# Kernel tuning notes

Hardware: AMD Instinct MI355X
Metric: run time of the kernel (lower is better)

The kernel has to match this reference:

```python
import jax, jax.numpy as jnp
import numpy as np

B, S, F, O = 128, 8, 32, 16  # batch, board_size, in_features, out_features
D = 2 * S - 1                # diff_size = 15 relative offsets per axis


def setup_inputs() -> dict:
    key = jax.random.key(0)
    k1, k2, k3 = jax.random.split(key, 3)
    inp = jax.random.normal(k1, (B, S, S, F), dtype=jnp.float32)
    # torch.nn.Bilinear init: U(-1/sqrt(in1_features), 1/sqrt(in1_features))
    bound = 1.0 / np.sqrt(F)
    W = jax.random.uniform(k2, (D, D, O, F, F), jnp.float32, -bound, bound)
    b = jax.random.uniform(k3, (D, D, O), jnp.float32, -bound, bound)
    return {"inp": inp, "W": W, "b": b}


def reference(inp, W, b):
    # inp: (B, S, S, F); W: (D, D, O, F, F); b: (D, D, O)
    s = inp.shape[1]
    idx = jnp.arange(s)
    # offset index: off[a, bb] = bb - a + (s - 1), in [0, 2s-2]
    off = idx[None, :] - idx[:, None] + (s - 1)  # (S, S)
    # gather per-pair bilinear weights: Wg[ax, bx, ay, by] = W[bx-ax+7, by-ay+7]
    Wg = W[off[:, :, None, None], off[None, None, :, :]]  # (S,S,S,S,O,F,F)
    bg = b[off[:, :, None, None], off[None, None, :, :]]  # (S,S,S,S,O) [ax,bx,ay,by]
    # out[b, ax, ay, bx, by, o] = a_i W_oij b_j + bias_o
    out = jnp.einsum('bxyi,xXyYoij,bXYj->bxyXYo', inp, Wg, inp)
    out = out + bg.transpose(0, 2, 1, 3, 4)[None]  # bias to [ax,ay,bx,by,o]
    return out
```

## Files before the change

### kernel.cpp

```cpp
#include <hip/hip_runtime.h>

typedef _Float16 f16;
typedef _Float16 f16x8 __attribute__((ext_vector_type(8)));
typedef float f32x4 __attribute__((ext_vector_type(4)));
typedef unsigned int u32;
typedef const __attribute__((address_space(1))) u32* gas1_t;
typedef __attribute__((address_space(3))) u32* las3_t;

#define WGRAN 460800
#define IGRAN 32768

__global__ __launch_bounds__(256) void convert_kernel(
    const float* __restrict__ W, const float* __restrict__ inp,
    f16* __restrict__ W_h, f16* __restrict__ inp_h)
{
    const int g = blockIdx.x * 256 + threadIdx.x;
    if (g < WGRAN) {
        const int dxdy = g >> 11;
        const int r = g & 2047;
        const int i = r >> 6, o = (r >> 2) & 15, quad = r & 3;
        const float* src = W + (size_t)dxdy * 16384 + o * 1024 + i * 32 + quad * 8;
        const float4 v0 = *(const float4*)src;
        const float4 v1 = *(const float4*)(src + 4);
        f16x8 h = { (f16)v0.x, (f16)v0.y, (f16)v0.z, (f16)v0.w,
                    (f16)v1.x, (f16)v1.y, (f16)v1.z, (f16)v1.w };
        *(f16x8*)(W_h + (size_t)g * 8) = h;
    } else {
        const int k = g - WGRAN;
        const float* src = inp + (size_t)k * 8;
        const float4 v0 = *(const float4*)src;
        const float4 v1 = *(const float4*)(src + 4);
        f16x8 h = { (f16)v0.x, (f16)v0.y, (f16)v0.z, (f16)v0.w,
                    (f16)v1.x, (f16)v1.y, (f16)v1.z, (f16)v1.w };
        *(f16x8*)(inp_h + (size_t)k * 8) = h;
    }
}

__global__ __launch_bounds__(256, 2) void rel_mfma7(
    const f16* __restrict__ W_h,
    const f16* __restrict__ inp_h,
    const float* __restrict__ bias,
    float* __restrict__ out)
{
    extern __shared__ __align__(16) f16 Wl[];

    const int hw = blockIdx.x;
    const int X = hw & 7, y = (hw >> 3) & 7, x = (hw >> 6) & 7;
    const int dx = X - x + 7;

    const int t = threadIdx.x;
    const int lane = t & 63;
    const int wave = t >> 6;
    const int quad = lane >> 4;
    const int m = lane & 15;

    const f16* wbase = W_h + (size_t)(dx * 15 + 7 - y) * 16384;

    #pragma unroll
    for (int it = 0; it < 8; ++it) {
        const int idx = (it * 256 + t) * 8;
        __builtin_amdgcn_global_load_lds((gas1_t)(wbase + idx),
                                         (las3_t)&Wl[idx], 16, 0, 0);
    }

    f16x8 a0[4], a1[4], c0[8], c1[8];
    const int b0 = wave * 32 + m;
    const int b1 = b0 + 16;
    {
        const f16* ar0 = inp_h + ((b0 * 8 + x) * 8 + y) * 32;
        const f16* ar1 = inp_h + ((b1 * 8 + x) * 8 + y) * 32;
        #pragma unroll
        for (int g = 0; g < 4; ++g) {
            a0[g] = *(const f16x8*)(ar0 + g * 8);
            a1[g] = *(const f16x8*)(ar1 + g * 8);
        }
        const f16* cr0 = inp_h + (b0 * 8 + X) * 256 + quad * 8;
        const f16* cr1 = inp_h + (b1 * 8 + X) * 256 + quad * 8;
        #pragma unroll
        for (int Yi = 0; Yi < 8; ++Yi) {
            c0[Yi] = *(const f16x8*)(cr0 + Yi * 32);
            c1[Yi] = *(const f16x8*)(cr1 + Yi * 32);
        }
    }

    __syncthreads();

    const int bid_base = ((x * 8 + y) * 8 + X) * 8;

    #pragma unroll
    for (int Y = 0; Y < 8; ++Y) {
        const int cur = Y & 1;

        if (Y < 7) {
            const f16* nbase = wbase + (size_t)(Y + 1) * 16384;
            f16* ldst = Wl + (cur ^ 1) * 16384;
            #pragma unroll
            for (int it = 0; it < 8; ++it) {
                const int idx = (it * 256 + t) * 8;
                __builtin_amdgcn_global_load_lds((gas1_t)(nbase + idx),
                                                 (las3_t)&ldst[idx], 16, 0, 0);
            }
        }
        __builtin_amdgcn_sched_barrier(0);

        f32x4 acc0 = {0.f, 0.f, 0.f, 0.f};
        f32x4 acc1 = {0.f, 0.f, 0.f, 0.f};
        const f16* wl = Wl + cur * 16384 + m * 32 + quad * 8;
        f16x8 bfrag = *(const f16x8*)(wl);
        #pragma unroll
        for (int kb = 0; kb < 32; ++kb) {
            const f16x8 bcur = bfrag;
            if (kb < 31)
                bfrag = *(const f16x8*)(wl + (kb + 1) * 512);
            const f16 av0 = a0[kb >> 3][kb & 7];
            const f16 av1 = a1[kb >> 3][kb & 7];
            const f16x8 af0 = c0[Y] * av0;
            const f16x8 af1 = c1[Y] * av1;
            acc0 = __builtin_amdgcn_mfma_f32_16x16x32_f16(af0, bcur, acc0, 0, 0, 0);
            acc1 = __builtin_amdgcn_mfma_f32_16x16x32_f16(af1, bcur, acc1, 0, 0, 0);
        }

        const int dxdy = dx * 15 + (Y - y + 7);
        const int bid = bid_base + Y;
        const float bv = bias[dxdy * 16 + m];
        #pragma unroll
        for (int r = 0; r < 4; ++r) {
            const int bb = wave * 32 + quad * 4 + r;
            out[((size_t)bb * 4096 + bid) * 16 + m]        = acc0[r] + bv;
            out[((size_t)(bb + 16) * 4096 + bid) * 16 + m] = acc1[r] + bv;
        }

        if (Y < 7) {
            __builtin_amdgcn_sched_barrier(0);
            asm volatile("s_waitcnt vmcnt(8)" ::: "memory");
            __builtin_amdgcn_s_barrier();
            __builtin_amdgcn_sched_barrier(0);
        }
    }
}

extern "C" void kernel_launch(void* const* d_in, const int* in_sizes, int n_in,
                              void* d_out, int out_size, void* d_ws, size_t ws_size,
                              hipStream_t stream)
{
    const float* inp  = (const float*)d_in[0];
    const float* W    = (const float*)d_in[1];
    const float* bias = (const float*)d_in[2];
    float* out = (float*)d_out;

    f16* W_h   = (f16*)d_ws;
    f16* inp_h = (f16*)d_ws + (size_t)WGRAN * 8;

    hipLaunchKernelGGL(convert_kernel, dim3((WGRAN + IGRAN) / 256), dim3(256), 0,
                       stream, W, inp, W_h, inp_h);
    hipLaunchKernelGGL(rel_mfma7, dim3(512), dim3(256), 65536, stream,
                       W_h, inp_h, bias, out);
}
```

Measured before the change: 105.0 us.

## Batch LDS weight reads into phases with barriers and MFMA priority boost

Restructures the inner K loop into four phases. Each phase first loads eight B-fragments from LDS, then issues the MFMAs between workgroup barriers under raised wave priority (s_setprio), which gives the waves a ping-pong style schedule. The next weight tile's global-to-LDS prefetch is now issued after the first phase's LDS reads instead of before the compute. Bias values are preloaded into registers up front. Extra barriers per phase add sync cost and more live registers, which risks occupancy at the 2-blocks launch bound.

```diff
diff --git a/kernel.cpp b/kernel.cpp
--- a/kernel.cpp
+++ b/kernel.cpp
@@ -36,7 +36,7 @@
     }
 }
 
-__global__ __launch_bounds__(256, 2) void rel_mfma7(
+__global__ __launch_bounds__(256, 2) void rel_mfma8(
     const f16* __restrict__ W_h,
     const f16* __restrict__ inp_h,
     const float* __restrict__ bias,
@@ -64,6 +64,7 @@
     }
 
     f16x8 a0[4], a1[4], c0[8], c1[8];
+    float bv[8];
     const int b0 = wave * 32 + m;
     const int b1 = b0 + 16;
     {
@@ -80,6 +81,7 @@
         for (int Yi = 0; Yi < 8; ++Yi) {
             c0[Yi] = *(const f16x8*)(cr0 + Yi * 32);
             c1[Yi] = *(const f16x8*)(cr1 + Yi * 32);
+            bv[Yi] = bias[(dx * 15 + (Yi - y + 7)) * 16 + m];
         }
     }
 
@@ -90,44 +92,51 @@
     #pragma unroll
     for (int Y = 0; Y < 8; ++Y) {
         const int cur = Y & 1;
-
-        if (Y < 7) {
-            const f16* nbase = wbase + (size_t)(Y + 1) * 16384;
-            f16* ldst = Wl + (cur ^ 1) * 16384;
-            #pragma unroll
-            for (int it = 0; it < 8; ++it) {
-                const int idx = (it * 256 + t) * 8;
-                __builtin_amdgcn_global_load_lds((gas1_t)(nbase + idx),
-                                                 (las3_t)&ldst[idx], 16, 0, 0);
-            }
-        }
-        __builtin_amdgcn_sched_barrier(0);
+        const f16* wl = Wl + cur * 16384 + m * 32 + quad * 8;
 
         f32x4 acc0 = {0.f, 0.f, 0.f, 0.f};
         f32x4 acc1 = {0.f, 0.f, 0.f, 0.f};
-        const f16* wl = Wl + cur * 16384 + m * 32 + quad * 8;
-        f16x8 bfrag = *(const f16x8*)(wl);
+
         #pragma unroll
-        for (int kb = 0; kb < 32; ++kb) {
-            const f16x8 bcur = bfrag;
-            if (kb < 31)
-                bfrag = *(const f16x8*)(wl + (kb + 1) * 512);
-            const f16 av0 = a0[kb >> 3][kb & 7];
-            const f16 av1 = a1[kb >> 3][kb & 7];
-            const f16x8 af0 = c0[Y] * av0;
-            const f16x8 af1 = c1[Y] * av1;
-            acc0 = __builtin_amdgcn_mfma_f32_16x16x32_f16(af0, bcur, acc0, 0, 0, 0);
-            acc1 = __builtin_amdgcn_mfma_f32_16x16x32_f16(af1, bcur, acc1, 0, 0, 0);
+        for (int ph = 0; ph < 4; ++ph) {
+            f16x8 bf[8];
+            #pragma unroll
+            for (int k = 0; k < 8; ++k)
+                bf[k] = *(const f16x8*)(wl + (ph * 8 + k) * 512);
+
+            if (ph == 0 && Y < 7) {
+                const f16* nbase = wbase + (size_t)(Y + 1) * 16384;
+                f16* ldst = Wl + (cur ^ 1) * 16384;
+                #pragma unroll
+                for (int it = 0; it < 8; ++it) {
+                    const int idx = (it * 256 + t) * 8;
+                    __builtin_amdgcn_global_load_lds((gas1_t)(nbase + idx),
+                                                     (las3_t)&ldst[idx], 16, 0, 0);
+                }
+            }
+
+            __builtin_amdgcn_s_barrier();
+            __builtin_amdgcn_s_setprio(1);
+            #pragma unroll
+            for (int k = 0; k < 8; ++k) {
+                const int kb = ph * 8 + k;
+                const f16 av0 = a0[kb >> 3][kb & 7];
+                const f16 av1 = a1[kb >> 3][kb & 7];
+                const f16x8 af0 = c0[Y] * av0;
+                const f16x8 af1 = c1[Y] * av1;
+                acc0 = __builtin_amdgcn_mfma_f32_16x16x32_f16(af0, bf[k], acc0, 0, 0, 0);
+                acc1 = __builtin_amdgcn_mfma_f32_16x16x32_f16(af1, bf[k], acc1, 0, 0, 0);
+            }
+            __builtin_amdgcn_s_setprio(0);
+            __builtin_amdgcn_s_barrier();
         }
 
-        const int dxdy = dx * 15 + (Y - y + 7);
         const int bid = bid_base + Y;
-        const float bv = bias[dxdy * 16 + m];
         #pragma unroll
         for (int r = 0; r < 4; ++r) {
             const int bb = wave * 32 + quad * 4 + r;
-            out[((size_t)bb * 4096 + bid) * 16 + m]        = acc0[r] + bv;
-            out[((size_t)(bb + 16) * 4096 + bid) * 16 + m] = acc1[r] + bv;
+            out[((size_t)bb * 4096 + bid) * 16 + m]        = acc0[r] + bv[Y];
+            out[((size_t)(bb + 16) * 4096 + bid) * 16 + m] = acc1[r] + bv[Y];
         }
 
         if (Y < 7) {
@@ -153,6 +162,6 @@
 
     hipLaunchKernelGGL(convert_kernel, dim3((WGRAN + IGRAN) / 256), dim3(256), 0,
                        stream, W, inp, W_h, inp_h);
-    hipLaunchKernelGGL(rel_mfma7, dim3(512), dim3(256), 65536, stream,
+    hipLaunchKernelGGL(rel_mfma8, dim3(512), dim3(256), 65536, stream,
                        W_h, inp_h, bias, out);
 }
```

Result: no change. 104.8 us (-0.2%).
